# Kernel tuning notes

Measured on AMD Instinct MI355X. Metric: run time of the kernel, lower is better.

The kernel has to match this reference:

```python
import jax, jax.numpy as jnp
import numpy as np

H = 128      # hidden_dim
ED = 16      # edge_dim
N = 50000    # n_nodes
E = 500000   # n_edges
B = 1
EPS = 1e-5


def setup_inputs() -> dict:
    key = jax.random.key(0)
    ks = jax.random.split(key, 16)
    s = 0.02
    inp = {
        "h": jax.random.normal(ks[0], (B, N, H), jnp.float32),
        "edge_attr": jax.random.normal(ks[1], (B, E, ED), jnp.float32),
        "edge_index": jax.random.randint(ks[2], (E, 2), 0, N, jnp.int32),
        # src_proj
        "src_W": jax.random.normal(ks[3], (H, H), jnp.float32) * s,
        "src_b": jnp.zeros((H,), jnp.float32),
        # edge_net: Linear(2H+ED -> H), GELU, Linear(H -> 2H)
        "e1_W": jax.random.normal(ks[4], (2 * H + ED, H), jnp.float32) * s,
        "e1_b": jnp.zeros((H,), jnp.float32),
        "e2_W": jax.random.normal(ks[5], (H, 2 * H), jnp.float32) * s,
        "e2_b": jnp.zeros((2 * H,), jnp.float32),
        # self_proj / agg_proj
        "self_W": jax.random.normal(ks[6], (H, H), jnp.float32) * s,
        "self_b": jnp.zeros((H,), jnp.float32),
        "agg_W": jax.random.normal(ks[7], (H, H), jnp.float32) * s,
        "agg_b": jnp.zeros((H,), jnp.float32),
        # LayerNorm
        "ln_g": jnp.ones((H,), jnp.float32),
        "ln_b": jnp.zeros((H,), jnp.float32),
    }
    return inp


def reference(h, edge_attr, edge_index, src_W, src_b, e1_W, e1_b, e2_W, e2_b,
              self_W, self_b, agg_W, agg_b, ln_g, ln_b):
    src = edge_index[:, 0]
    dst = edge_index[:, 1]

    h_src = h[:, src, :]                      # [B, E, H]
    h_dst = h[:, dst, :]                      # [B, E, H]
    edge_input = jnp.concatenate([h_src, h_dst, edge_attr], axis=-1)  # [B, E, 2H+ED]

    hid = jax.nn.gelu(edge_input @ e1_W + e1_b, approximate=False)    # [B, E, H]
    edge_ctx = hid @ e2_W + e2_b                                      # [B, E, 2H]
    gate, shift = jnp.split(edge_ctx, 2, axis=-1)
    msg = jax.nn.sigmoid(gate) * (h_src @ src_W + src_b) + shift      # [B, E, H]

    # scatter-add over destination nodes
    agg = jnp.zeros_like(h).at[:, dst, :].add(msg)                    # [B, N, H]
    indeg = jnp.maximum(jnp.zeros((N,), h.dtype).at[dst].add(1.0), 1.0)
    agg = agg / indeg[None, :, None]

    update = (h @ self_W + self_b) + (agg @ agg_W + agg_b)
    x = h + jax.nn.gelu(update, approximate=False)

    mu = jnp.mean(x, axis=-1, keepdims=True)
    var = jnp.var(x, axis=-1, keepdims=True)
    return (x - mu) / jnp.sqrt(var + EPS) * ln_g + ln_b
```

## Files before the change

kernel.cpp:

```cpp
#include <hip/hip_runtime.h>
#include <hip/hip_bf16.h>
#include <math.h>

#define HD 128
#define NN 50000
#define NE 500000
#define LN_EPS 1e-5f

typedef __attribute__((ext_vector_type(8))) short short8;
typedef __attribute__((ext_vector_type(4))) float f32x4;

__device__ __forceinline__ unsigned short f2bf(float f) {
    unsigned int u = __float_as_uint(f);
    u = (u + 0x7FFFu + ((u >> 16) & 1u)) >> 16;
    return (unsigned short)u;
}
__device__ __forceinline__ float bf2f(unsigned short b) {
    return __uint_as_float(((unsigned int)b) << 16);
}
__device__ __forceinline__ float gelu_f(float x) {
    return 0.5f * x * (1.0f + erff(x * 0.70710678118654752440f));
}
__device__ __forceinline__ float sigm_f(float x) {
    return 1.0f / (1.0f + __expf(-x));
}

__global__ __launch_bounds__(384) void node_pre_kernel(
    const float* __restrict__ h,
    const float* __restrict__ src_W, const float* __restrict__ src_b,
    const float* __restrict__ e1_W, const float* __restrict__ e1_b,
    unsigned short* __restrict__ hswb,
    unsigned short* __restrict__ a1b,
    unsigned short* __restrict__ b1b)
{
    const int lane = threadIdx.x & 63;
    const int w = threadIdx.x >> 6;
    const int lo = lane & 15, hi = lane >> 4;
    const int m0 = blockIdx.x * 64;

    short8 bf[4][4];
    #pragma unroll
    for (int nn = 0; nn < 4; ++nn) {
        const int c = w * 64 + nn * 16 + lo;
        #pragma unroll
        for (int kk = 0; kk < 4; ++kk) {
            short8 v;
            #pragma unroll
            for (int j = 0; j < 8; ++j) {
                const int k = kk * 32 + hi * 8 + j;
                float wv;
                if (c < 128)      wv = src_W[k * 128 + c];
                else if (c < 256) wv = e1_W[k * 128 + (c - 128)];
                else              wv = e1_W[(128 + k) * 128 + (c - 256)];
                v[j] = (short)f2bf(wv);
            }
            bf[kk][nn] = v;
        }
    }

    f32x4 acc[4][4];
    #pragma unroll
    for (int mm = 0; mm < 4; ++mm)
        #pragma unroll
        for (int nn = 0; nn < 4; ++nn)
            acc[mm][nn] = (f32x4){0.f, 0.f, 0.f, 0.f};

    #pragma unroll
    for (int mm = 0; mm < 4; ++mm) {
        int row = m0 + mm * 16 + lo;
        if (row >= NN) row = NN - 1;
        short8 af[4];
        #pragma unroll
        for (int kk = 0; kk < 4; ++kk) {
            const float* p = h + row * 128 + kk * 32 + hi * 8;
            short8 v;
            #pragma unroll
            for (int j = 0; j < 8; ++j) v[j] = (short)f2bf(p[j]);
            af[kk] = v;
        }
        #pragma unroll
        for (int nn = 0; nn < 4; ++nn)
            #pragma unroll
            for (int kk = 0; kk < 4; ++kk)
                acc[mm][nn] = __builtin_amdgcn_mfma_f32_16x16x32_bf16(
                    af[kk], bf[kk][nn], acc[mm][nn], 0, 0, 0);
    }

    #pragma unroll
    for (int mm = 0; mm < 4; ++mm) {
        #pragma unroll
        for (int nn = 0; nn < 4; ++nn) {
            const int c = w * 64 + nn * 16 + lo;
            #pragma unroll
            for (int r = 0; r < 4; ++r) {
                const int row = m0 + mm * 16 + hi * 4 + r;
                if (row < NN) {
                    const float v = acc[mm][nn][r];
                    if (c < 128)      hswb[row * 128 + c]       = f2bf(v + src_b[c]);
                    else if (c < 256) a1b [row * 128 + (c-128)] = f2bf(v + e1_b[c-128]);
                    else              b1b [row * 128 + (c-256)] = f2bf(v);
                }
            }
        }
    }
}

__global__ __launch_bounds__(256, 2) void edge_kernel(
    const float* __restrict__ edge_attr, const int* __restrict__ edge_index,
    const float* __restrict__ e1_W, const float* __restrict__ e2_W, const float* __restrict__ e2_b,
    const unsigned short* __restrict__ hswb,
    const unsigned short* __restrict__ a1b, const unsigned short* __restrict__ b1b,
    float* __restrict__ agg, float* __restrict__ indeg, int nblocks)
{
    __shared__ unsigned int hid32[64 * 64];
    __shared__ int src_lds[64];
    __shared__ int dst_lds[64];

    const int lane = threadIdx.x & 63;
    const int w = __builtin_amdgcn_readfirstlane(threadIdx.x >> 6);
    const int lo = lane & 15, hi = lane >> 4;

    float e1c0[16], e1c1[16];
    #pragma unroll
    for (int k = 0; k < 16; ++k) {
        e1c0[k] = e1_W[(256 + k) * 128 + 2 * lane];
        e1c1[k] = e1_W[(256 + k) * 128 + 2 * lane + 1];
    }

    short8 bf[4][4];
    #pragma unroll
    for (int nn = 0; nn < 4; ++nn) {
        const int nbase = (nn < 2) ? (w * 32 + nn * 16) : (128 + w * 32 + (nn - 2) * 16);
        const int n = nbase + lo;
        #pragma unroll
        for (int kk = 0; kk < 4; ++kk) {
            short8 v;
            #pragma unroll
            for (int j = 0; j < 8; ++j) {
                const int k = kk * 32 + hi * 8 + j;
                v[j] = (short)f2bf(e2_W[k * 256 + n]);
            }
            bf[kk][nn] = v;
        }
    }
    float bg[2], bs[2];
    #pragma unroll
    for (int nn = 0; nn < 2; ++nn) {
        bg[nn] = e2_b[w * 32 + nn * 16 + lo];
        bs[nn] = e2_b[128 + w * 32 + nn * 16 + lo];
    }

    for (int eb = blockIdx.x; eb < nblocks; eb += gridDim.x) {
        for (int ee = 0; ee < 16; ++ee) {
            const int er = w * 16 + ee;
            const int e = eb * 64 + er;
            if (e < NE) {
                const int s = edge_index[2 * e];
                const int d = edge_index[2 * e + 1];
                if (lane == 0) {
                    src_lds[er] = s;
                    dst_lds[er] = d;
                    unsafeAtomicAdd(&indeg[d], 1.0f);
                }
                const unsigned int av = *(const unsigned int*)(a1b + s * 128 + 2 * lane);
                const unsigned int bv = *(const unsigned int*)(b1b + d * 128 + 2 * lane);
                float t0 = bf2f((unsigned short)(av & 0xFFFFu)) + bf2f((unsigned short)(bv & 0xFFFFu));
                float t1 = bf2f((unsigned short)(av >> 16))     + bf2f((unsigned short)(bv >> 16));
                #pragma unroll
                for (int k = 0; k < 16; ++k) {
                    const float ea = edge_attr[e * 16 + k];
                    t0 += ea * e1c0[k];
                    t1 += ea * e1c1[k];
                }
                t0 = gelu_f(t0);
                t1 = gelu_f(t1);
                const unsigned int hv = (unsigned int)f2bf(t0) | ((unsigned int)f2bf(t1) << 16);
                const int chunk = (lane >> 2) ^ (er & 7);
                hid32[er * 64 + chunk * 4 + (lane & 3)] = hv;
            }
        }
        __syncthreads();

        f32x4 acc[4][4];
        #pragma unroll
        for (int mm = 0; mm < 4; ++mm)
            #pragma unroll
            for (int nn = 0; nn < 4; ++nn)
                acc[mm][nn] = (f32x4){0.f, 0.f, 0.f, 0.f};

        #pragma unroll
        for (int mm = 0; mm < 4; ++mm) {
            const int row = mm * 16 + lo;
            short8 af[4];
            #pragma unroll
            for (int kk = 0; kk < 4; ++kk) {
                const int sb = ((kk * 4 + hi) ^ (row & 7)) << 4;
                af[kk] = *(const short8*)((const char*)hid32 + row * 256 + sb);
            }
            #pragma unroll
            for (int nn = 0; nn < 4; ++nn)
                #pragma unroll
                for (int kk = 0; kk < 4; ++kk)
                    acc[mm][nn] = __builtin_amdgcn_mfma_f32_16x16x32_bf16(
                        af[kk], bf[kk][nn], acc[mm][nn], 0, 0, 0);
        }

        #pragma unroll
        for (int mm = 0; mm < 4; ++mm) {
            #pragma unroll
            for (int r = 0; r < 4; ++r) {
                const int er = mm * 16 + hi * 4 + r;
                const int e = eb * 64 + er;
                if (e < NE) {
                    const int s = src_lds[er];
                    const int d = dst_lds[er];
                    #pragma unroll
                    for (int nn = 0; nn < 2; ++nn) {
                        const int c = w * 32 + nn * 16 + lo;
                        const float g  = acc[mm][nn][r]     + bg[nn];
                        const float sh = acc[mm][nn + 2][r] + bs[nn];
                        const float hv = bf2f(hswb[s * 128 + c]);
                        const float msg = sigm_f(g) * hv + sh;
                        unsafeAtomicAdd(&agg[d * 128 + c], msg);
                    }
                }
            }
        }
        __syncthreads();
    }
}

__global__ __launch_bounds__(256) void node_post_kernel(
    const float* __restrict__ h,
    const float* __restrict__ self_W, const float* __restrict__ self_b,
    const float* __restrict__ agg_W, const float* __restrict__ agg_b,
    const float* __restrict__ ln_g, const float* __restrict__ ln_b,
    const float* __restrict__ agg, const float* __restrict__ indeg,
    float* __restrict__ out)
{
    __shared__ float x_lds[64 * 129];
    const int lane = threadIdx.x & 63;
    const int w = threadIdx.x >> 6;
    const int lo = lane & 15, hi = lane >> 4;
    const int m0 = blockIdx.x * 64;

    short8 bf[8][2];
    #pragma unroll
    for (int nn = 0; nn < 2; ++nn) {
        const int c = w * 32 + nn * 16 + lo;
        #pragma unroll
        for (int kk = 0; kk < 8; ++kk) {
            short8 v;
            #pragma unroll
            for (int j = 0; j < 8; ++j) {
                const int k = kk * 32 + hi * 8 + j;
                const float wv = (k < 128) ? self_W[k * 128 + c] : agg_W[(k - 128) * 128 + c];
                v[j] = (short)f2bf(wv);
            }
            bf[kk][nn] = v;
        }
    }

    f32x4 acc[4][2];
    #pragma unroll
    for (int mm = 0; mm < 4; ++mm)
        #pragma unroll
        for (int nn = 0; nn < 2; ++nn)
            acc[mm][nn] = (f32x4){0.f, 0.f, 0.f, 0.f};

    #pragma unroll
    for (int mm = 0; mm < 4; ++mm) {
        int row = m0 + mm * 16 + lo;
        if (row >= NN) row = NN - 1;
        const float rdeg = 1.0f / fmaxf(indeg[row], 1.0f);
        short8 af[8];
        #pragma unroll
        for (int kk = 0; kk < 4; ++kk) {
            const float* p = h + row * 128 + kk * 32 + hi * 8;
            short8 v;
            #pragma unroll
            for (int j = 0; j < 8; ++j) v[j] = (short)f2bf(p[j]);
            af[kk] = v;
        }
        #pragma unroll
        for (int kk = 4; kk < 8; ++kk) {
            const float* p = agg + row * 128 + (kk - 4) * 32 + hi * 8;
            short8 v;
            #pragma unroll
            for (int j = 0; j < 8; ++j) v[j] = (short)f2bf(p[j] * rdeg);
            af[kk] = v;
        }
        #pragma unroll
        for (int nn = 0; nn < 2; ++nn)
            #pragma unroll
            for (int kk = 0; kk < 8; ++kk)
                acc[mm][nn] = __builtin_amdgcn_mfma_f32_16x16x32_bf16(
                    af[kk], bf[kk][nn], acc[mm][nn], 0, 0, 0);
    }

    #pragma unroll
    for (int mm = 0; mm < 4; ++mm) {
        #pragma unroll
        for (int nn = 0; nn < 2; ++nn) {
            const int c = w * 32 + nn * 16 + lo;
            const float bsum = self_b[c] + agg_b[c];
            #pragma unroll
            for (int r = 0; r < 4; ++r) {
                const int rl = mm * 16 + hi * 4 + r;
                int row = m0 + rl;
                if (row >= NN) row = NN - 1;
                const float upd = acc[mm][nn][r] + bsum;
                const float xv = h[row * 128 + c] + gelu_f(upd);
                x_lds[rl * 129 + c] = xv;
            }
        }
    }
    __syncthreads();

    const int rrow = threadIdx.x >> 2;
    const int part = threadIdx.x & 3;
    float sum = 0.f, ss = 0.f;
    #pragma unroll
    for (int i = 0; i < 32; ++i) {
        const float v = x_lds[rrow * 129 + part * 32 + i];
        sum += v; ss += v * v;
    }
    sum += __shfl_xor(sum, 1); ss += __shfl_xor(ss, 1);
    sum += __shfl_xor(sum, 2); ss += __shfl_xor(ss, 2);
    const float mu = sum * (1.0f / 128.0f);
    const float var = ss * (1.0f / 128.0f) - mu * mu;
    const float rstd = rsqrtf(var + LN_EPS);
    const int grow = m0 + rrow;
    if (grow < NN) {
        #pragma unroll
        for (int i = 0; i < 32; ++i) {
            const int c = part * 32 + i;
            const float v = x_lds[rrow * 129 + c];
            out[grow * 128 + c] = (v - mu) * rstd * ln_g[c] + ln_b[c];
        }
    }
}

extern "C" void kernel_launch(void* const* d_in, const int* in_sizes, int n_in,
                              void* d_out, int out_size, void* d_ws, size_t ws_size,
                              hipStream_t stream) {
    const float* h         = (const float*)d_in[0];
    const float* edge_attr = (const float*)d_in[1];
    const int*   edge_index= (const int*)  d_in[2];
    const float* src_W     = (const float*)d_in[3];
    const float* src_b     = (const float*)d_in[4];
    const float* e1_W      = (const float*)d_in[5];
    const float* e1_b      = (const float*)d_in[6];
    const float* e2_W      = (const float*)d_in[7];
    const float* e2_b      = (const float*)d_in[8];
    const float* self_W    = (const float*)d_in[9];
    const float* self_b    = (const float*)d_in[10];
    const float* agg_W     = (const float*)d_in[11];
    const float* agg_b     = (const float*)d_in[12];
    const float* ln_g      = (const float*)d_in[13];
    const float* ln_b      = (const float*)d_in[14];
    float* out = (float*)d_out;

    char* ws = (char*)d_ws;
    unsigned short* hswb = (unsigned short*)(ws);
    unsigned short* a1b  = (unsigned short*)(ws + 12800000);
    unsigned short* b1b  = (unsigned short*)(ws + 25600000);
    float* agg   = (float*)(ws + 38400000);
    float* indeg = (float*)(ws + 64000000);

    hipMemsetAsync(agg, 0, 25600000 + 200000, stream);

    node_pre_kernel<<<(NN + 63) / 64, 384, 0, stream>>>(
        h, src_W, src_b, e1_W, e1_b, hswb, a1b, b1b);

    const int nblocks = (NE + 63) / 64;
    edge_kernel<<<2608, 256, 0, stream>>>(
        edge_attr, edge_index, e1_W, e2_W, e2_b, hswb, a1b, b1b, agg, indeg, nblocks);

    node_post_kernel<<<(NN + 63) / 64, 256, 0, stream>>>(
        h, self_W, self_b, agg_W, agg_b, ln_g, ln_b, agg, indeg, out);
}
```

Baseline: 723.0 us.

## Sort edges by destination and pre-reduce messages in shared memory before global atomics

Adds a counting sort of edge ids by destination (histogram, single-block scan, scatter) and has the edge kernel walk edges in sorted order. It merges runs with the same destination in registers and an LDS tile, then issues one global atomic per distinct destination and column. The aim is to cut the heavy global float atomic traffic on the aggregate buffer. Node kernels also become grid-stride with float4 loads, the edge_attr loads are vectorised, and the in-degree comes from the integer histogram. The cost is three extra launches, a serial single-block scan, and gathers of src, dst and edge_attr through an indirection.

```diff
diff --git a/kernel.cpp b/kernel.cpp
--- a/kernel.cpp
+++ b/kernel.cpp
@@ -36,7 +36,6 @@
     const int lane = threadIdx.x & 63;
     const int w = threadIdx.x >> 6;
     const int lo = lane & 15, hi = lane >> 4;
-    const int m0 = blockIdx.x * 64;
 
     short8 bf[4][4];
     #pragma unroll
@@ -58,63 +57,123 @@
         }
     }
 
-    f32x4 acc[4][4];
-    #pragma unroll
-    for (int mm = 0; mm < 4; ++mm)
-        #pragma unroll
-        for (int nn = 0; nn < 4; ++nn)
-            acc[mm][nn] = (f32x4){0.f, 0.f, 0.f, 0.f};
-
-    #pragma unroll
-    for (int mm = 0; mm < 4; ++mm) {
-        int row = m0 + mm * 16 + lo;
-        if (row >= NN) row = NN - 1;
-        short8 af[4];
-        #pragma unroll
-        for (int kk = 0; kk < 4; ++kk) {
-            const float* p = h + row * 128 + kk * 32 + hi * 8;
-            short8 v;
-            #pragma unroll
-            for (int j = 0; j < 8; ++j) v[j] = (short)f2bf(p[j]);
-            af[kk] = v;
-        }
-        #pragma unroll
-        for (int nn = 0; nn < 4; ++nn)
-            #pragma unroll
-            for (int kk = 0; kk < 4; ++kk)
-                acc[mm][nn] = __builtin_amdgcn_mfma_f32_16x16x32_bf16(
-                    af[kk], bf[kk][nn], acc[mm][nn], 0, 0, 0);
-    }
-
-    #pragma unroll
-    for (int mm = 0; mm < 4; ++mm) {
-        #pragma unroll
-        for (int nn = 0; nn < 4; ++nn) {
-            const int c = w * 64 + nn * 16 + lo;
-            #pragma unroll
-            for (int r = 0; r < 4; ++r) {
-                const int row = m0 + mm * 16 + hi * 4 + r;
-                if (row < NN) {
-                    const float v = acc[mm][nn][r];
-                    if (c < 128)      hswb[row * 128 + c]       = f2bf(v + src_b[c]);
-                    else if (c < 256) a1b [row * 128 + (c-128)] = f2bf(v + e1_b[c-128]);
-                    else              b1b [row * 128 + (c-256)] = f2bf(v);
+    for (int m0 = blockIdx.x * 64; m0 < NN; m0 += gridDim.x * 64) {
+        f32x4 acc[4][4];
+        #pragma unroll
+        for (int mm = 0; mm < 4; ++mm)
+            #pragma unroll
+            for (int nn = 0; nn < 4; ++nn)
+                acc[mm][nn] = (f32x4){0.f, 0.f, 0.f, 0.f};
+
+        #pragma unroll
+        for (int mm = 0; mm < 4; ++mm) {
+            int row = m0 + mm * 16 + lo;
+            if (row >= NN) row = NN - 1;
+            short8 af[4];
+            #pragma unroll
+            for (int kk = 0; kk < 4; ++kk) {
+                const float* p = h + row * 128 + kk * 32 + hi * 8;
+                const float4 q0 = *(const float4*)p;
+                const float4 q1 = *(const float4*)(p + 4);
+                short8 v;
+                v[0] = (short)f2bf(q0.x); v[1] = (short)f2bf(q0.y);
+                v[2] = (short)f2bf(q0.z); v[3] = (short)f2bf(q0.w);
+                v[4] = (short)f2bf(q1.x); v[5] = (short)f2bf(q1.y);
+                v[6] = (short)f2bf(q1.z); v[7] = (short)f2bf(q1.w);
+                af[kk] = v;
+            }
+            #pragma unroll
+            for (int nn = 0; nn < 4; ++nn)
+                #pragma unroll
+                for (int kk = 0; kk < 4; ++kk)
+                    acc[mm][nn] = __builtin_amdgcn_mfma_f32_16x16x32_bf16(
+                        af[kk], bf[kk][nn], acc[mm][nn], 0, 0, 0);
+        }
+
+        #pragma unroll
+        for (int mm = 0; mm < 4; ++mm) {
+            #pragma unroll
+            for (int nn = 0; nn < 4; ++nn) {
+                const int c = w * 64 + nn * 16 + lo;
+                #pragma unroll
+                for (int r = 0; r < 4; ++r) {
+                    const int row = m0 + mm * 16 + hi * 4 + r;
+                    if (row < NN) {
+                        const float v = acc[mm][nn][r];
+                        if (c < 128)      hswb[row * 128 + c]       = f2bf(v + src_b[c]);
+                        else if (c < 256) a1b [row * 128 + (c-128)] = f2bf(v + e1_b[c-128]);
+                        else              b1b [row * 128 + (c-256)] = f2bf(v);
+                    }
                 }
             }
         }
+    }
+}
+
+__global__ __launch_bounds__(256) void hist_kernel(
+    const int* __restrict__ edge_index, int* __restrict__ deg)
+{
+    const int e = blockIdx.x * 256 + threadIdx.x;
+    if (e < NE) atomicAdd(&deg[edge_index[2 * e + 1]], 1);
+}
+
+__global__ __launch_bounds__(1024) void scan_kernel(
+    const int* __restrict__ deg, int* __restrict__ cursor)
+{
+    __shared__ int sums[1024];
+    const int t = threadIdx.x;
+    const int chunk = (NN + 1023) / 1024;
+    const int i0 = t * chunk;
+    int s = 0;
+    for (int i = 0; i < chunk; ++i) {
+        const int idx = i0 + i;
+        if (idx < NN) s += deg[idx];
+    }
+    sums[t] = s;
+    __syncthreads();
+    for (int off = 1; off < 1024; off <<= 1) {
+        const int v = (t >= off) ? sums[t - off] : 0;
+        __syncthreads();
+        sums[t] += v;
+        __syncthreads();
+    }
+    int run = (t > 0) ? sums[t - 1] : 0;
+    for (int i = 0; i < chunk; ++i) {
+        const int idx = i0 + i;
+        if (idx < NN) {
+            cursor[idx] = run;
+            run += deg[idx];
+        }
+    }
+}
+
+__global__ __launch_bounds__(256) void scatter_kernel(
+    const int* __restrict__ edge_index, int* __restrict__ cursor,
+    int* __restrict__ sorted_eid)
+{
+    const int e = blockIdx.x * 256 + threadIdx.x;
+    if (e < NE) {
+        const int d = edge_index[2 * e + 1];
+        const int pos = atomicAdd(&cursor[d], 1);
+        sorted_eid[pos] = e;
     }
 }
 
 __global__ __launch_bounds__(256, 2) void edge_kernel(
     const float* __restrict__ edge_attr, const int* __restrict__ edge_index,
+    const int* __restrict__ sorted_eid,
     const float* __restrict__ e1_W, const float* __restrict__ e2_W, const float* __restrict__ e2_b,
     const unsigned short* __restrict__ hswb,
     const unsigned short* __restrict__ a1b, const unsigned short* __restrict__ b1b,
-    float* __restrict__ agg, float* __restrict__ indeg, int nblocks)
+    float* __restrict__ agg, int nblocks)
 {
     __shared__ unsigned int hid32[64 * 64];
+    __shared__ float agg_tile[64 * 128];
     __shared__ int src_lds[64];
     __shared__ int dst_lds[64];
+    __shared__ int lid_lds[64];
+    __shared__ int gdst_lds[64];
+    __shared__ int ndist_lds;
 
     const int lane = threadIdx.x & 63;
     const int w = __builtin_amdgcn_readfirstlane(threadIdx.x >> 6);
@@ -150,36 +209,56 @@
         bs[nn] = e2_b[128 + w * 32 + nn * 16 + lo];
     }
 
+    for (int i = threadIdx.x; i < 64 * 128; i += 256) agg_tile[i] = 0.f;
+
     for (int eb = blockIdx.x; eb < nblocks; eb += gridDim.x) {
         for (int ee = 0; ee < 16; ++ee) {
             const int er = w * 16 + ee;
-            const int e = eb * 64 + er;
-            if (e < NE) {
-                const int s = edge_index[2 * e];
-                const int d = edge_index[2 * e + 1];
-                if (lane == 0) {
-                    src_lds[er] = s;
-                    dst_lds[er] = d;
-                    unsafeAtomicAdd(&indeg[d], 1.0f);
-                }
+            const int ti = eb * 64 + er;
+            if (ti < NE) {
+                const int eid = sorted_eid[ti];
+                const int s = edge_index[2 * eid];
+                const int d = edge_index[2 * eid + 1];
+                if (lane == 0) { src_lds[er] = s; dst_lds[er] = d; }
                 const unsigned int av = *(const unsigned int*)(a1b + s * 128 + 2 * lane);
                 const unsigned int bv = *(const unsigned int*)(b1b + d * 128 + 2 * lane);
                 float t0 = bf2f((unsigned short)(av & 0xFFFFu)) + bf2f((unsigned short)(bv & 0xFFFFu));
                 float t1 = bf2f((unsigned short)(av >> 16))     + bf2f((unsigned short)(bv >> 16));
+                const float4 q0 = *(const float4*)(edge_attr + eid * 16);
+                const float4 q1 = *(const float4*)(edge_attr + eid * 16 + 4);
+                const float4 q2 = *(const float4*)(edge_attr + eid * 16 + 8);
+                const float4 q3 = *(const float4*)(edge_attr + eid * 16 + 12);
+                const float ea[16] = {q0.x,q0.y,q0.z,q0.w, q1.x,q1.y,q1.z,q1.w,
+                                      q2.x,q2.y,q2.z,q2.w, q3.x,q3.y,q3.z,q3.w};
                 #pragma unroll
                 for (int k = 0; k < 16; ++k) {
-                    const float ea = edge_attr[e * 16 + k];
-                    t0 += ea * e1c0[k];
-                    t1 += ea * e1c1[k];
+                    t0 += ea[k] * e1c0[k];
+                    t1 += ea[k] * e1c1[k];
                 }
                 t0 = gelu_f(t0);
                 t1 = gelu_f(t1);
                 const unsigned int hv = (unsigned int)f2bf(t0) | ((unsigned int)f2bf(t1) << 16);
                 const int chunk = (lane >> 2) ^ (er & 7);
                 hid32[er * 64 + chunk * 4 + (lane & 3)] = hv;
-            }
-        }
-        __syncthreads();
+            } else if (lane == 0) {
+                dst_lds[er] = -1;
+            }
+        }
+        __syncthreads();
+
+        if (w == 0) {
+            const int er = lane;
+            const int d = dst_lds[er];
+            const bool valid = (eb * 64 + er < NE);
+            const bool flag = valid && (er == 0 || dst_lds[er - 1] != d);
+            const unsigned long long mask = __ballot(flag ? 1 : 0);
+            const unsigned long long below =
+                (er == 63) ? mask : (mask & ((1ull << (er + 1)) - 1ull));
+            const int lid = (int)__popcll(below) - 1;
+            lid_lds[er] = lid;
+            if (flag) gdst_lds[lid] = d;
+            if (er == 0) ndist_lds = (int)__popcll(mask);
+        }
 
         f32x4 acc[4][4];
         #pragma unroll
@@ -204,29 +283,42 @@
                     acc[mm][nn] = __builtin_amdgcn_mfma_f32_16x16x32_bf16(
                         af[kk], bf[kk][nn], acc[mm][nn], 0, 0, 0);
         }
-
-        #pragma unroll
-        for (int mm = 0; mm < 4; ++mm) {
-            #pragma unroll
-            for (int r = 0; r < 4; ++r) {
-                const int er = mm * 16 + hi * 4 + r;
-                const int e = eb * 64 + er;
-                if (e < NE) {
-                    const int s = src_lds[er];
-                    const int d = dst_lds[er];
-                    #pragma unroll
-                    for (int nn = 0; nn < 2; ++nn) {
-                        const int c = w * 32 + nn * 16 + lo;
+        __syncthreads();
+
+        #pragma unroll
+        for (int mm = 0; mm < 4; ++mm) {
+            #pragma unroll
+            for (int nn = 0; nn < 2; ++nn) {
+                const int c = w * 32 + nn * 16 + lo;
+                float pend = 0.f;
+                int plid = -1;
+                #pragma unroll
+                for (int r = 0; r < 4; ++r) {
+                    const int er = mm * 16 + hi * 4 + r;
+                    if (eb * 64 + er < NE) {
+                        const int s = src_lds[er];
                         const float g  = acc[mm][nn][r]     + bg[nn];
                         const float sh = acc[mm][nn + 2][r] + bs[nn];
-                        const float hv = bf2f(hswb[s * 128 + c]);
-                        const float msg = sigm_f(g) * hv + sh;
-                        unsafeAtomicAdd(&agg[d * 128 + c], msg);
+                        const float msg = sigm_f(g) * bf2f(hswb[s * 128 + c]) + sh;
+                        const int lid = lid_lds[er];
+                        if (lid != plid) {
+                            if (plid >= 0) atomicAdd(&agg_tile[plid * 128 + c], pend);
+                            plid = lid; pend = 0.f;
+                        }
+                        pend += msg;
                     }
                 }
-            }
-        }
-        __syncthreads();
+                if (plid >= 0) atomicAdd(&agg_tile[plid * 128 + c], pend);
+            }
+        }
+        __syncthreads();
+
+        const int nd = ndist_lds;
+        for (int i = threadIdx.x; i < nd * 128; i += 256) {
+            const float v = agg_tile[i];
+            agg_tile[i] = 0.f;
+            unsafeAtomicAdd(&agg[gdst_lds[i >> 7] * 128 + (i & 127)], v);
+        }
     }
 }
 
@@ -235,14 +327,13 @@
     const float* __restrict__ self_W, const float* __restrict__ self_b,
     const float* __restrict__ agg_W, const float* __restrict__ agg_b,
     const float* __restrict__ ln_g, const float* __restrict__ ln_b,
-    const float* __restrict__ agg, const float* __restrict__ indeg,
+    const float* __restrict__ agg, const int* __restrict__ deg,
     float* __restrict__ out)
 {
     __shared__ float x_lds[64 * 129];
     const int lane = threadIdx.x & 63;
     const int w = threadIdx.x >> 6;
     const int lo = lane & 15, hi = lane >> 4;
-    const int m0 = blockIdx.x * 64;
 
     short8 bf[8][2];
     #pragma unroll
@@ -261,83 +352,93 @@
         }
     }
 
-    f32x4 acc[4][2];
-    #pragma unroll
-    for (int mm = 0; mm < 4; ++mm)
-        #pragma unroll
-        for (int nn = 0; nn < 2; ++nn)
-            acc[mm][nn] = (f32x4){0.f, 0.f, 0.f, 0.f};
-
-    #pragma unroll
-    for (int mm = 0; mm < 4; ++mm) {
-        int row = m0 + mm * 16 + lo;
-        if (row >= NN) row = NN - 1;
-        const float rdeg = 1.0f / fmaxf(indeg[row], 1.0f);
-        short8 af[8];
-        #pragma unroll
-        for (int kk = 0; kk < 4; ++kk) {
-            const float* p = h + row * 128 + kk * 32 + hi * 8;
-            short8 v;
-            #pragma unroll
-            for (int j = 0; j < 8; ++j) v[j] = (short)f2bf(p[j]);
-            af[kk] = v;
-        }
-        #pragma unroll
-        for (int kk = 4; kk < 8; ++kk) {
-            const float* p = agg + row * 128 + (kk - 4) * 32 + hi * 8;
-            short8 v;
-            #pragma unroll
-            for (int j = 0; j < 8; ++j) v[j] = (short)f2bf(p[j] * rdeg);
-            af[kk] = v;
-        }
-        #pragma unroll
-        for (int nn = 0; nn < 2; ++nn)
-            #pragma unroll
-            for (int kk = 0; kk < 8; ++kk)
-                acc[mm][nn] = __builtin_amdgcn_mfma_f32_16x16x32_bf16(
-                    af[kk], bf[kk][nn], acc[mm][nn], 0, 0, 0);
-    }
-
-    #pragma unroll
-    for (int mm = 0; mm < 4; ++mm) {
-        #pragma unroll
-        for (int nn = 0; nn < 2; ++nn) {
-            const int c = w * 32 + nn * 16 + lo;
-            const float bsum = self_b[c] + agg_b[c];
-            #pragma unroll
-            for (int r = 0; r < 4; ++r) {
-                const int rl = mm * 16 + hi * 4 + r;
-                int row = m0 + rl;
-                if (row >= NN) row = NN - 1;
-                const float upd = acc[mm][nn][r] + bsum;
-                const float xv = h[row * 128 + c] + gelu_f(upd);
-                x_lds[rl * 129 + c] = xv;
-            }
-        }
-    }
-    __syncthreads();
-
-    const int rrow = threadIdx.x >> 2;
-    const int part = threadIdx.x & 3;
-    float sum = 0.f, ss = 0.f;
-    #pragma unroll
-    for (int i = 0; i < 32; ++i) {
-        const float v = x_lds[rrow * 129 + part * 32 + i];
-        sum += v; ss += v * v;
-    }
-    sum += __shfl_xor(sum, 1); ss += __shfl_xor(ss, 1);
-    sum += __shfl_xor(sum, 2); ss += __shfl_xor(ss, 2);
-    const float mu = sum * (1.0f / 128.0f);
-    const float var = ss * (1.0f / 128.0f) - mu * mu;
-    const float rstd = rsqrtf(var + LN_EPS);
-    const int grow = m0 + rrow;
-    if (grow < NN) {
+    for (int m0 = blockIdx.x * 64; m0 < NN; m0 += gridDim.x * 64) {
+        f32x4 acc[4][2];
+        #pragma unroll
+        for (int mm = 0; mm < 4; ++mm)
+            #pragma unroll
+            for (int nn = 0; nn < 2; ++nn)
+                acc[mm][nn] = (f32x4){0.f, 0.f, 0.f, 0.f};
+
+        #pragma unroll
+        for (int mm = 0; mm < 4; ++mm) {
+            int row = m0 + mm * 16 + lo;
+            if (row >= NN) row = NN - 1;
+            const float rdeg = 1.0f / fmaxf((float)deg[row], 1.0f);
+            short8 af[8];
+            #pragma unroll
+            for (int kk = 0; kk < 4; ++kk) {
+                const float* p = h + row * 128 + kk * 32 + hi * 8;
+                const float4 q0 = *(const float4*)p;
+                const float4 q1 = *(const float4*)(p + 4);
+                short8 v;
+                v[0] = (short)f2bf(q0.x); v[1] = (short)f2bf(q0.y);
+                v[2] = (short)f2bf(q0.z); v[3] = (short)f2bf(q0.w);
+                v[4] = (short)f2bf(q1.x); v[5] = (short)f2bf(q1.y);
+                v[6] = (short)f2bf(q1.z); v[7] = (short)f2bf(q1.w);
+                af[kk] = v;
+            }
+            #pragma unroll
+            for (int kk = 4; kk < 8; ++kk) {
+                const float* p = agg + row * 128 + (kk - 4) * 32 + hi * 8;
+                const float4 q0 = *(const float4*)p;
+                const float4 q1 = *(const float4*)(p + 4);
+                short8 v;
+                v[0] = (short)f2bf(q0.x * rdeg); v[1] = (short)f2bf(q0.y * rdeg);
+                v[2] = (short)f2bf(q0.z * rdeg); v[3] = (short)f2bf(q0.w * rdeg);
+                v[4] = (short)f2bf(q1.x * rdeg); v[5] = (short)f2bf(q1.y * rdeg);
+                v[6] = (short)f2bf(q1.z * rdeg); v[7] = (short)f2bf(q1.w * rdeg);
+                af[kk] = v;
+            }
+            #pragma unroll
+            for (int nn = 0; nn < 2; ++nn)
+                #pragma unroll
+                for (int kk = 0; kk < 8; ++kk)
+                    acc[mm][nn] = __builtin_amdgcn_mfma_f32_16x16x32_bf16(
+                        af[kk], bf[kk][nn], acc[mm][nn], 0, 0, 0);
+        }
+
+        #pragma unroll
+        for (int mm = 0; mm < 4; ++mm) {
+            #pragma unroll
+            for (int nn = 0; nn < 2; ++nn) {
+                const int c = w * 32 + nn * 16 + lo;
+                const float bsum = self_b[c] + agg_b[c];
+                #pragma unroll
+                for (int r = 0; r < 4; ++r) {
+                    const int rl = mm * 16 + hi * 4 + r;
+                    int row = m0 + rl;
+                    if (row >= NN) row = NN - 1;
+                    const float upd = acc[mm][nn][r] + bsum;
+                    x_lds[rl * 129 + c] = h[row * 128 + c] + gelu_f(upd);
+                }
+            }
+        }
+        __syncthreads();
+
+        const int rrow = threadIdx.x >> 2;
+        const int part = threadIdx.x & 3;
+        float sum = 0.f, ss = 0.f;
         #pragma unroll
         for (int i = 0; i < 32; ++i) {
-            const int c = part * 32 + i;
-            const float v = x_lds[rrow * 129 + c];
-            out[grow * 128 + c] = (v - mu) * rstd * ln_g[c] + ln_b[c];
-        }
+            const float v = x_lds[rrow * 129 + part * 32 + i];
+            sum += v; ss += v * v;
+        }
+        sum += __shfl_xor(sum, 1); ss += __shfl_xor(ss, 1);
+        sum += __shfl_xor(sum, 2); ss += __shfl_xor(ss, 2);
+        const float mu = sum * (1.0f / 128.0f);
+        const float var = ss * (1.0f / 128.0f) - mu * mu;
+        const float rstd = rsqrtf(var + LN_EPS);
+        const int grow = m0 + rrow;
+        if (grow < NN) {
+            #pragma unroll
+            for (int i = 0; i < 32; ++i) {
+                const int c = part * 32 + i;
+                const float v = x_lds[rrow * 129 + c];
+                out[grow * 128 + c] = (v - mu) * rstd * ln_g[c] + ln_b[c];
+            }
+        }
+        __syncthreads();
     }
 }
 
@@ -365,18 +466,25 @@
     unsigned short* hswb = (unsigned short*)(ws);
     unsigned short* a1b  = (unsigned short*)(ws + 12800000);
     unsigned short* b1b  = (unsigned short*)(ws + 25600000);
-    float* agg   = (float*)(ws + 38400000);
-    float* indeg = (float*)(ws + 64000000);
+    float* agg        = (float*)(ws + 38400000);
+    int*   deg        = (int*)  (ws + 64000000);
+    int*   cursor     = (int*)  (ws + 64200000);
+    int*   sorted_eid = (int*)  (ws + 64400000);
 
     hipMemsetAsync(agg, 0, 25600000 + 200000, stream);
 
-    node_pre_kernel<<<(NN + 63) / 64, 384, 0, stream>>>(
+    node_pre_kernel<<<256, 384, 0, stream>>>(
         h, src_W, src_b, e1_W, e1_b, hswb, a1b, b1b);
 
+    hist_kernel<<<(NE + 255) / 256, 256, 0, stream>>>(edge_index, deg);
+    scan_kernel<<<1, 1024, 0, stream>>>(deg, cursor);
+    scatter_kernel<<<(NE + 255) / 256, 256, 0, stream>>>(edge_index, cursor, sorted_eid);
+
     const int nblocks = (NE + 63) / 64;
-    edge_kernel<<<2608, 256, 0, stream>>>(
-        edge_attr, edge_index, e1_W, e2_W, e2_b, hswb, a1b, b1b, agg, indeg, nblocks);
-
-    node_post_kernel<<<(NN + 63) / 64, 256, 0, stream>>>(
-        h, self_W, self_b, agg_W, agg_b, ln_g, ln_b, agg, indeg, out);
-}
+    edge_kernel<<<1024, 256, 0, stream>>>(
+        edge_attr, edge_index, sorted_eid, e1_W, e2_W, e2_b,
+        hswb, a1b, b1b, agg, nblocks);
+
+    node_post_kernel<<<256, 256, 0, stream>>>(
+        h, self_W, self_b, agg_W, agg_b, ln_g, ln_b, agg, deg, out);
+}
```

Result: slower. 838.7 us (+16.0%).
